# Kernel optimization log

Measured on AMD Instinct MI355X. Metric: run time of the kernel, lower is better.

The kernel has to match this reference:

```python
import jax, jax.numpy as jnp
import numpy as np

B, N, CIN, H, OUT, L, K = 8, 512, 64, 64, 64, 256, 3
EPS = 1e-5


def setup_inputs() -> dict:
    key = jax.random.key(0)
    ks = jax.random.split(key, 12)
    def unif(k, shape, fan):
        s = 1.0 / np.sqrt(fan)
        return jax.random.uniform(k, shape, jnp.float32, -s, s)
    return {
        "x": jax.random.normal(ks[0], (B, N, CIN, L), jnp.float32),
        "adj": jax.random.uniform(ks[1], (B, N, N), jnp.float32),
        # temp_conv1: Conv1d(CIN->H, k=3)
        "w1": unif(ks[2], (H, CIN, K), CIN * K),
        "b1": unif(ks[3], (H,), CIN * K),
        # graph_conv: Linear-style (H,H) + bias, stdv=1/sqrt(out_features)
        "gw": unif(ks[4], (H, H), H),
        "gb": unif(ks[5], (H,), H),
        # temp_conv2: Conv1d(H->OUT, k=3)
        "w2": unif(ks[6], (OUT, H, K), H * K),
        "b2": unif(ks[7], (OUT,), H * K),
        # residual: Conv1d(CIN->OUT, k=1) == pointwise linear
        "wr": unif(ks[8], (OUT, CIN), CIN),
        "br": unif(ks[9], (OUT,), CIN),
        # BatchNorm2d(OUT) affine params
        "gamma": jnp.ones((OUT,), jnp.float32),
        "beta": jnp.zeros((OUT,), jnp.float32),
    }


def _conv1d(x, w, b, pad):
    # x: (B, N, C, L) -> flatten node dim into batch, NCH conv
    b_, n_, c, l = x.shape
    y = jax.lax.conv_general_dilated(
        x.reshape(b_ * n_, c, l), w, window_strides=(1,),
        padding=[(pad, pad)], dimension_numbers=("NCH", "OIH", "NCH"))
    y = y + b[None, :, None]
    return y.reshape(b_, n_, w.shape[0], l)


def reference(x, adj, w1, b1, gw, gb, w2, b2, wr, br, gamma, beta):
    pad = (K - 1) // 2
    # residual branch: 1x1 conv over channels
    residual = jnp.einsum("bncl,oc->bnol", x, wr) + br[None, None, :, None]
    # temporal conv 1
    out = _conv1d(x, w1, b1, pad)                      # (B,N,H,L)
    # graph conv over all timesteps at once (replaces per-t Python loop)
    xw = jnp.einsum("bnhl,hd->bndl", out, gw)          # (B,N,H,L)
    out = jnp.einsum("bnm,bmdl->bndl", adj, xw) + gb[None, None, :, None]
    # temporal conv 2
    out = _conv1d(out, w2, b2, pad)                    # (B,N,OUT,L)
    out = out + residual
    # BatchNorm2d over channel axis (training-mode batch stats, biased var)
    mean = jnp.mean(out, axis=(0, 1, 3), keepdims=True)
    var = jnp.mean(jnp.square(out - mean), axis=(0, 1, 3), keepdims=True)
    out = (out - mean) * jax.lax.rsqrt(var + EPS)
    out = out * gamma[None, None, :, None] + beta[None, None, :, None]
    return jax.nn.relu(out)
```

## Files before the change

### kernel.cpp

```cpp
#include <hip/hip_runtime.h>
#include <hip/hip_bf16.h>
#include <stdint.h>


typedef unsigned short u16;
typedef unsigned int   u32;
typedef __attribute__((ext_vector_type(8))) short           bf16x8;
typedef __attribute__((ext_vector_type(8))) unsigned short  u16x8;
typedef __attribute__((ext_vector_type(4))) unsigned short  u16x4;
typedef __attribute__((ext_vector_type(4))) float           f32x4;

__device__ __forceinline__ float bf2f(u16 v){
  union { u32 u; float f; } x; x.u = ((u32)v) << 16; return x.f;
}
__device__ __forceinline__ u16 f2bf(float f){
  __hip_bfloat16 h = __float2bfloat16(f);
  return *reinterpret_cast<u16*>(&h);
}
__device__ __forceinline__ u32 swz(int row, int cbyte){
  return (u32)(row * 128) + (u32)(cbyte ^ ((row & 7) << 4));
}

__device__ __forceinline__ void stage_Tf(const float* __restrict__ src, u16* dst, int t){
  const int c0 = (t & 31) * 2;
  const int l0 = (t >> 5) * 32;
  #pragma unroll
  for (int v = 0; v < 8; ++v){
    f32x4 a = *(const f32x4*)(src + (size_t)c0 * 256 + l0 + v * 4);
    f32x4 b = *(const f32x4*)(src + (size_t)(c0 + 1) * 256 + l0 + v * 4);
    #pragma unroll
    for (int e = 0; e < 4; ++e){
      u32 p = (u32)f2bf(a[e]) | ((u32)f2bf(b[e]) << 16);
      *(u32*)((char*)dst + swz(l0 + v * 4 + e, c0 * 2)) = p;
    }
  }
}
__device__ __forceinline__ void stage_Tb(const u16* __restrict__ src, u16* dst, int t){
  const int c0 = (t & 31) * 2;
  const int l0 = (t >> 5) * 32;
  #pragma unroll
  for (int v = 0; v < 4; ++v){
    u16x8 a = *(const u16x8*)(src + (size_t)c0 * 256 + l0 + v * 8);
    u16x8 b = *(const u16x8*)(src + (size_t)(c0 + 1) * 256 + l0 + v * 8);
    #pragma unroll
    for (int e = 0; e < 8; ++e){
      u32 p = (u32)a[e] | ((u32)b[e] << 16);
      *(u32*)((char*)dst + swz(l0 + v * 8 + e, c0 * 2)) = p;
    }
  }
}

__global__ __launch_bounds__(256) void k_prep(const float* __restrict__ w1, const float* __restrict__ gw,
    const float* __restrict__ w2, const float* __restrict__ wr,
    u16* __restrict__ w1t, u16* __restrict__ gwt, u16* __restrict__ w2t, u16* __restrict__ wrt){
  int t = threadIdx.x;
  for (int e = t; e < 12288; e += 256){
    int tap = e >> 12, rem = e & 4095, o = rem >> 6, c = rem & 63;
    w1t[e] = f2bf(w1[(o * 64 + c) * 3 + tap]);
    w2t[e] = f2bf(w2[(o * 64 + c) * 3 + tap]);
  }
  for (int e = t; e < 4096; e += 256){
    int d = e >> 6, h = e & 63;
    gwt[e] = f2bf(gw[h * 64 + d]);
    wrt[e] = f2bf(wr[e]);
  }
}

__global__ __launch_bounds__(256) void k_p1(const float* __restrict__ x,
    const u16* __restrict__ w1t, const float* __restrict__ b1v,
    const u16* __restrict__ gwt, const u16* __restrict__ wrt,
    u16* __restrict__ outA, u16* __restrict__ outR){
  __shared__ u16 tile[16384];
  const int t = threadIdx.x;
  const size_t bn = (size_t)blockIdx.x + (size_t)blockIdx.y * 512;
  stage_Tf(x + bn * 16384, tile, t);
  __syncthreads();
  const int w = t >> 6, ln = t & 63, lq = ln >> 4, lr = ln & 15;
  const bf16x8 z8 = {};

  {
    f32x4 racc[4][4];
    #pragma unroll
    for (int i = 0; i < 4; ++i)
      #pragma unroll
      for (int j = 0; j < 4; ++j) racc[i][j] = (f32x4){0.f, 0.f, 0.f, 0.f};
    #pragma unroll
    for (int kk = 0; kk < 2; ++kk){
      bf16x8 A[4];
      #pragma unroll
      for (int fo = 0; fo < 4; ++fo)
        A[fo] = *(const bf16x8*)(wrt + (fo * 16 + lr) * 64 + kk * 32 + lq * 8);
      #pragma unroll
      for (int fc = 0; fc < 4; ++fc){
        int l = w * 64 + fc * 16 + lr;
        bf16x8 B = *(const bf16x8*)((char*)tile + swz(l, kk * 64 + lq * 16));
        #pragma unroll
        for (int fo = 0; fo < 4; ++fo)
          racc[fo][fc] = __builtin_amdgcn_mfma_f32_16x16x32_bf16(A[fo], B, racc[fo][fc], 0, 0, 0);
      }
    }
    u16* rp = outR + bn * 16384 + t * 64;
    #pragma unroll
    for (int v = 0; v < 8; ++v){
      u16x8 ov;
      const int fo = v >> 1;
      #pragma unroll
      for (int h = 0; h < 2; ++h){
        const int fc = (v & 1) * 2 + h;
        #pragma unroll
        for (int r2 = 0; r2 < 4; ++r2)
          ov[h * 4 + r2] = f2bf(racc[fo][fc][r2]);
      }
      *(u16x8*)(rp + v * 8) = ov;
    }
  }

  f32x4 acc[4][4];
  #pragma unroll
  for (int i = 0; i < 4; ++i)
    #pragma unroll
    for (int j = 0; j < 4; ++j) acc[i][j] = (f32x4){0.f, 0.f, 0.f, 0.f};
  #pragma unroll
  for (int tap = 0; tap < 3; ++tap){
    #pragma unroll
    for (int kk = 0; kk < 2; ++kk){
      bf16x8 A[4];
      #pragma unroll
      for (int fo = 0; fo < 4; ++fo)
        A[fo] = *(const bf16x8*)(w1t + tap * 4096 + (fo * 16 + lr) * 64 + kk * 32 + lq * 8);
      #pragma unroll
      for (int fc = 0; fc < 4; ++fc){
        int r = w * 64 + fc * 16 + lr + tap - 1;
        int rc = r < 0 ? 0 : (r > 255 ? 255 : r);
        bf16x8 B = *(const bf16x8*)((char*)tile + swz(rc, kk * 64 + lq * 16));
        if (r != rc) B = z8;
        #pragma unroll
        for (int fo = 0; fo < 4; ++fo)
          acc[fo][fc] = __builtin_amdgcn_mfma_f32_16x16x32_bf16(A[fo], B, acc[fo][fc], 0, 0, 0);
      }
    }
  }
  __syncthreads();
  #pragma unroll
  for (int fo = 0; fo < 4; ++fo){
    float b0 = b1v[fo * 16 + lq * 4 + 0];
    float b1_ = b1v[fo * 16 + lq * 4 + 1];
    float b2_ = b1v[fo * 16 + lq * 4 + 2];
    float b3 = b1v[fo * 16 + lq * 4 + 3];
    #pragma unroll
    for (int fc = 0; fc < 4; ++fc){
      int l = w * 64 + fc * 16 + lr;
      u32 p0 = (u32)f2bf(acc[fo][fc][0] + b0) | ((u32)f2bf(acc[fo][fc][1] + b1_) << 16);
      u32 p1 = (u32)f2bf(acc[fo][fc][2] + b2_) | ((u32)f2bf(acc[fo][fc][3] + b3) << 16);
      char* p = (char*)tile + swz(l, fo * 32 + lq * 8);
      *(u32*)p = p0;
      *(u32*)(p + 4) = p1;
    }
  }
  f32x4 acc2[4][4];
  #pragma unroll
  for (int i = 0; i < 4; ++i)
    #pragma unroll
    for (int j = 0; j < 4; ++j) acc2[i][j] = (f32x4){0.f, 0.f, 0.f, 0.f};
  #pragma unroll
  for (int kk = 0; kk < 2; ++kk){
    bf16x8 A[4];
    #pragma unroll
    for (int fo = 0; fo < 4; ++fo)
      A[fo] = *(const bf16x8*)(gwt + (fo * 16 + lr) * 64 + kk * 32 + lq * 8);
    #pragma unroll
    for (int fc = 0; fc < 4; ++fc){
      int l = w * 64 + fc * 16 + lr;
      bf16x8 B = *(const bf16x8*)((char*)tile + swz(l, kk * 64 + lq * 16));
      #pragma unroll
      for (int fo = 0; fo < 4; ++fo)
        acc2[fo][fc] = __builtin_amdgcn_mfma_f32_16x16x32_bf16(A[fo], B, acc2[fo][fc], 0, 0, 0);
    }
  }
  u16* op = outA + bn * 16384;
  #pragma unroll
  for (int fo = 0; fo < 4; ++fo)
    #pragma unroll
    for (int fc = 0; fc < 4; ++fc){
      int l = w * 64 + fc * 16 + lr;
      #pragma unroll
      for (int r2 = 0; r2 < 4; ++r2)
        op[(fo * 16 + lq * 4 + r2) * 256 + l] = f2bf(acc2[fo][fc][r2]);
    }
}

__global__ __launch_bounds__(256) void k_p3(const u16* __restrict__ xw,
    const float* __restrict__ adj, const float* __restrict__ gbv, u16* __restrict__ outB){
  __shared__ u16 At[8192];
  __shared__ u16 Bt[8192];
  const int t = threadIdx.x;
  const int jt = blockIdx.x, nt = blockIdx.y, b = blockIdx.z;
  const float* adjb = adj + ((size_t)b * 512 + (size_t)nt * 128) * 512;
  const u16* Xb = xw + (size_t)b * 8388608 + (size_t)jt * 128;
  const int w = t >> 6, ln = t & 63, lq = ln >> 4, lr = ln & 15;
  const int wrow = w >> 1, wcol = w & 1;
  const int mpair = t & 31, jq = t >> 5;
  f32x4 acc[4][4];
  #pragma unroll
  for (int i = 0; i < 4; ++i)
    #pragma unroll
    for (int j = 0; j < 4; ++j) acc[i][j] = (f32x4){0.f, 0.f, 0.f, 0.f};

  for (int ks = 0; ks < 8; ++ks){
    #pragma unroll
    for (int it = 0; it < 8; ++it){
      int c = it * 256 + t;
      int row = c >> 4, mc = c & 15;
      f32x4 v = *(const f32x4*)(adjb + (size_t)row * 512 + ks * 64 + mc * 4);
      u16x4 pk;
      #pragma unroll
      for (int e = 0; e < 4; ++e) pk[e] = f2bf(v[e]);
      *(u16x4*)((char*)At + (u32)(row * 128) + (u32)((mc * 8) ^ ((row & 7) << 4))) = pk;
    }
    {
      const u16* s0 = Xb + (size_t)(ks * 64 + mpair * 2) * 16384 + jq * 16;
      const u16* s1 = s0 + 16384;
      #pragma unroll
      for (int v2 = 0; v2 < 2; ++v2){
        u16x8 a = *(const u16x8*)(s0 + v2 * 8);
        u16x8 bb = *(const u16x8*)(s1 + v2 * 8);
        #pragma unroll
        for (int e = 0; e < 8; ++e){
          u32 p = (u32)a[e] | ((u32)bb[e] << 16);
          *(u32*)((char*)Bt + swz(jq * 16 + v2 * 8 + e, mpair * 4)) = p;
        }
      }
    }
    __syncthreads();
    #pragma unroll
    for (int kk = 0; kk < 2; ++kk){
      bf16x8 Af[4], Bf[4];
      #pragma unroll
      for (int f = 0; f < 4; ++f){
        int ra = wrow * 64 + f * 16 + lr;
        Af[f] = *(const bf16x8*)((char*)At + swz(ra, kk * 64 + lq * 16));
        int rb = wcol * 64 + f * 16 + lr;
        Bf[f] = *(const bf16x8*)((char*)Bt + swz(rb, kk * 64 + lq * 16));
      }
      #pragma unroll
      for (int fr = 0; fr < 4; ++fr)
        #pragma unroll
        for (int fc = 0; fc < 4; ++fc)
          acc[fr][fc] = __builtin_amdgcn_mfma_f32_16x16x32_bf16(Af[fr], Bf[fc], acc[fr][fc], 0, 0, 0);
    }
    __syncthreads();
  }
  const float gb = gbv[jt >> 1];
  u16* ob = outB + ((size_t)b * 512 + (size_t)nt * 128) * 16384 + (size_t)jt * 128;
  #pragma unroll
  for (int fr = 0; fr < 4; ++fr)
    #pragma unroll
    for (int fc = 0; fc < 4; ++fc)
      #pragma unroll
      for (int r2 = 0; r2 < 4; ++r2){
        int n_ = wrow * 64 + fr * 16 + lq * 4 + r2;
        int j_ = wcol * 64 + fc * 16 + lr;
        ob[(size_t)n_ * 16384 + j_] = f2bf(acc[fr][fc][r2] + gb);
      }
}

__global__ __launch_bounds__(256) void k_p4(const u16* __restrict__ g,
    const u16* __restrict__ resv, const u16* __restrict__ w2t,
    const float* __restrict__ b2v, const float* __restrict__ brv,
    u16* __restrict__ outP, float* __restrict__ spart){
  __shared__ u16 gt[16384];
  const int t = threadIdx.x;
  const size_t bn = (size_t)blockIdx.x + (size_t)blockIdx.y * 512;
  stage_Tb(g + bn * 16384, gt, t);
  __syncthreads();
  const int w = t >> 6, ln = t & 63, lq = ln >> 4, lr = ln & 15;
  const bf16x8 z8 = {};
  f32x4 acc[4][4];
  #pragma unroll
  for (int i = 0; i < 4; ++i)
    #pragma unroll
    for (int j = 0; j < 4; ++j) acc[i][j] = (f32x4){0.f, 0.f, 0.f, 0.f};

  #pragma unroll
  for (int tap = 0; tap < 3; ++tap){
    #pragma unroll
    for (int kk = 0; kk < 2; ++kk){
      bf16x8 A[4];
      #pragma unroll
      for (int fo = 0; fo < 4; ++fo)
        A[fo] = *(const bf16x8*)(w2t + tap * 4096 + (fo * 16 + lr) * 64 + kk * 32 + lq * 8);
      #pragma unroll
      for (int fc = 0; fc < 4; ++fc){
        int r = w * 64 + fc * 16 + lr + tap - 1;
        int rc = r < 0 ? 0 : (r > 255 ? 255 : r);
        bf16x8 B = *(const bf16x8*)((char*)gt + swz(rc, kk * 64 + lq * 16));
        if (r != rc) B = z8;
        #pragma unroll
        for (int fo = 0; fo < 4; ++fo)
          acc[fo][fc] = __builtin_amdgcn_mfma_f32_16x16x32_bf16(A[fo], B, acc[fo][fc], 0, 0, 0);
      }
    }
  }

  float bball[16];
  #pragma unroll
  for (int fo = 0; fo < 4; ++fo)
    #pragma unroll
    for (int r2 = 0; r2 < 4; ++r2){
      int o = fo * 16 + lq * 4 + r2;
      bball[fo * 4 + r2] = b2v[o] + brv[o];
    }
  float psum[16], psq[16];
  #pragma unroll
  for (int i = 0; i < 16; ++i){ psum[i] = 0.f; psq[i] = 0.f; }

  const u16* rp = resv + bn * 16384 + t * 64;
  u16x8 rv[8];
  #pragma unroll
  for (int v = 0; v < 8; ++v) rv[v] = *(const u16x8*)(rp + v * 8);

  u16* op = outP + bn * 16384;
  #pragma unroll
  for (int fo = 0; fo < 4; ++fo){
    #pragma unroll
    for (int fc = 0; fc < 4; ++fc){
      int l = w * 64 + fc * 16 + lr;
      #pragma unroll
      for (int r2 = 0; r2 < 4; ++r2){
        float val = acc[fo][fc][r2] + bball[fo * 4 + r2]
                  + bf2f(rv[fo * 2 + (fc >> 1)][(fc & 1) * 4 + r2]);
        op[(fo * 16 + lq * 4 + r2) * 256 + l] = f2bf(val);
        psum[fo * 4 + r2] += val;
        psq[fo * 4 + r2] += val * val;
      }
    }
  }

  #pragma unroll
  for (int i = 0; i < 16; ++i){
    #pragma unroll
    for (int m = 1; m < 16; m <<= 1){
      psum[i] += __shfl_xor(psum[i], m, 64);
      psq[i]  += __shfl_xor(psq[i],  m, 64);
    }
  }
  __syncthreads();
  float* sc = (float*)gt;
  if (lr == 0){
    #pragma unroll
    for (int i = 0; i < 16; ++i){
      int o = (i >> 2) * 16 + lq * 4 + (i & 3);
      sc[w * 128 + o]      = psum[i];
      sc[w * 128 + 64 + o] = psq[i];
    }
  }
  __syncthreads();
  if (t < 128){
    float tot = sc[t] + sc[128 + t] + sc[256 + t] + sc[384 + t];
    spart[(size_t)t * 4096 + bn] = tot;
  }
}

__global__ __launch_bounds__(256) void k_p5(const float* __restrict__ part, float* __restrict__ fin){
  const int o = blockIdx.x, t = threadIdx.x;
  float s1 = 0.f, s2 = 0.f;
  for (int k = t; k < 4096; k += 256){
    s1 += part[(size_t)o * 4096 + k];
    s2 += part[(size_t)(64 + o) * 4096 + k];
  }
  #pragma unroll
  for (int m = 32; m; m >>= 1){
    s1 += __shfl_down(s1, m, 64);
    s2 += __shfl_down(s2, m, 64);
  }
  __shared__ float red[8];
  if ((t & 63) == 0){ red[(t >> 6) * 2] = s1; red[(t >> 6) * 2 + 1] = s2; }
  __syncthreads();
  if (t == 0){
    float S1 = red[0] + red[2] + red[4] + red[6];
    float S2 = red[1] + red[3] + red[5] + red[7];
    const float invN = 1.f / 1048576.f;
    float mean = S1 * invN;
    float var = S2 * invN - mean * mean;
    fin[o] = mean;
    fin[64 + o] = rsqrtf(var + 1e-5f);
  }
}

__global__ __launch_bounds__(256) void k_p6(const u16* __restrict__ pre, const float* __restrict__ fin,
    const float* __restrict__ gamma, const float* __restrict__ beta, float* __restrict__ out){
  __shared__ float ssca[64], soff[64];
  const int tt = threadIdx.x;
  if (tt < 64){
    float sc = fin[64 + tt] * gamma[tt];
    ssca[tt] = sc;
    soff[tt] = beta[tt] - fin[tt] * sc;
  }
  __syncthreads();
  const size_t nchunk = 8388608;
  for (size_t i = (size_t)blockIdx.x * 256 + tt; i < nchunk; i += (size_t)gridDim.x * 256){
    int o = (int)((i >> 5) & 63);
    float sca = ssca[o], off = soff[o];
    u16x8 v = *(const u16x8*)(pre + i * 8);
    f32x4 oa, ob;
    #pragma unroll
    for (int e = 0; e < 4; ++e){
      float f0 = bf2f(v[e]) * sca + off;
      float f1 = bf2f(v[4 + e]) * sca + off;
      oa[e] = f0 > 0.f ? f0 : 0.f;
      ob[e] = f1 > 0.f ? f1 : 0.f;
    }
    *(f32x4*)(out + i * 8)     = oa;
    *(f32x4*)(out + i * 8 + 4) = ob;
  }
}

extern "C" void kernel_launch(void* const* d_in, const int* in_sizes, int n_in,
                              void* d_out, int out_size, void* d_ws, size_t ws_size,
                              hipStream_t stream){
  const float* x     = (const float*)d_in[0];
  const float* adj   = (const float*)d_in[1];
  const float* w1    = (const float*)d_in[2];
  const float* b1    = (const float*)d_in[3];
  const float* gw    = (const float*)d_in[4];
  const float* gb    = (const float*)d_in[5];
  const float* w2    = (const float*)d_in[6];
  const float* b2    = (const float*)d_in[7];
  const float* wr    = (const float*)d_in[8];
  const float* br    = (const float*)d_in[9];
  const float* gamma = (const float*)d_in[10];
  const float* beta  = (const float*)d_in[11];
  (void)in_sizes; (void)n_in; (void)out_size; (void)ws_size;

  char* ws = (char*)d_ws;
  u16*   bufA  = (u16*)ws;
  float* spart = (float*)(ws + 134217728);
  float* sfin  = (float*)(ws + 136314880);
  u16*   w1t   = (u16*)(ws + 136315392);
  u16*   gwt   = (u16*)(ws + 136339968);
  u16*   w2t   = (u16*)(ws + 136348160);
  u16*   wrt   = (u16*)(ws + 136372736);
  u16*   gbuf  = (u16*)d_out;
  u16*   bufR  = (u16*)d_out + 67108864;

  k_prep<<<1, 256, 0, stream>>>(w1, gw, w2, wr, w1t, gwt, w2t, wrt);
  k_p1<<<dim3(512, 8, 1), 256, 0, stream>>>(x, w1t, b1, gwt, wrt, bufA, bufR);
  k_p3<<<dim3(128, 4, 8), 256, 0, stream>>>(bufA, adj, gb, gbuf);
  k_p4<<<dim3(512, 8, 1), 256, 0, stream>>>(gbuf, bufR, w2t, b2, br, bufA, spart);
  k_p5<<<64, 256, 0, stream>>>(spart, sfin);
  k_p6<<<2048, 256, 0, stream>>>(bufA, sfin, gamma, beta, (float*)d_out);
}
```

Before: 587.7 us.

## Fold graph weight into conv1 weights and prefetch adjacency GEMM tiles

Precomputes gw^T·w1 per tap and b1·gw in the prep kernel, so k_p1 no longer needs its second GEMM, shared-memory round trip or extra barrier. The prep kernel now runs on 16 blocks. The adjacency GEMM kernel gets a flattened grid with a remapped block index to change scheduling locality across XCDs. It also prefetches the next K-slice of adj and xw into registers while the current slice is being multiplied. Folding the weights changes the rounding point (one bf16 rounding instead of two), and the prefetch raises register pressure.

```diff
diff --git a/kernel.cpp b/kernel.cpp
--- a/kernel.cpp
+++ b/kernel.cpp
@@ -50,26 +50,29 @@
   }
 }
 
-__global__ __launch_bounds__(256) void k_prep(const float* __restrict__ w1, const float* __restrict__ gw,
-    const float* __restrict__ w2, const float* __restrict__ wr,
-    u16* __restrict__ w1t, u16* __restrict__ gwt, u16* __restrict__ w2t, u16* __restrict__ wrt){
-  int t = threadIdx.x;
-  for (int e = t; e < 12288; e += 256){
+__global__ __launch_bounds__(256) void k_prep(const float* __restrict__ w1, const float* __restrict__ b1,
+    const float* __restrict__ gw, const float* __restrict__ w2, const float* __restrict__ wr,
+    u16* __restrict__ w1g, float* __restrict__ b1g, u16* __restrict__ w2t, u16* __restrict__ wrt){
+  const int gt = blockIdx.x * 256 + threadIdx.x, gs = gridDim.x * 256;
+  for (int e = gt; e < 12288; e += gs){
     int tap = e >> 12, rem = e & 4095, o = rem >> 6, c = rem & 63;
-    w1t[e] = f2bf(w1[(o * 64 + c) * 3 + tap]);
     w2t[e] = f2bf(w2[(o * 64 + c) * 3 + tap]);
-  }
-  for (int e = t; e < 4096; e += 256){
-    int d = e >> 6, h = e & 63;
-    gwt[e] = f2bf(gw[h * 64 + d]);
-    wrt[e] = f2bf(wr[e]);
+    float s = 0.f;
+    for (int h = 0; h < 64; ++h)
+      s += gw[h * 64 + o] * w1[(h * 64 + c) * 3 + tap];
+    w1g[e] = f2bf(s);
+  }
+  for (int e = gt; e < 4096; e += gs) wrt[e] = f2bf(wr[e]);
+  for (int d = gt; d < 64; d += gs){
+    float s = 0.f;
+    for (int h = 0; h < 64; ++h) s += b1[h] * gw[h * 64 + d];
+    b1g[d] = s;
   }
 }
 
 __global__ __launch_bounds__(256) void k_p1(const float* __restrict__ x,
-    const u16* __restrict__ w1t, const float* __restrict__ b1v,
-    const u16* __restrict__ gwt, const u16* __restrict__ wrt,
-    u16* __restrict__ outA, u16* __restrict__ outR){
+    const u16* __restrict__ w1g, const float* __restrict__ b1g,
+    const u16* __restrict__ wrt, u16* __restrict__ outA, u16* __restrict__ outR){
   __shared__ u16 tile[16384];
   const int t = threadIdx.x;
   const size_t bn = (size_t)blockIdx.x + (size_t)blockIdx.y * 512;
@@ -127,7 +130,7 @@
       bf16x8 A[4];
       #pragma unroll
       for (int fo = 0; fo < 4; ++fo)
-        A[fo] = *(const bf16x8*)(w1t + tap * 4096 + (fo * 16 + lr) * 64 + kk * 32 + lq * 8);
+        A[fo] = *(const bf16x8*)(w1g + tap * 4096 + (fo * 16 + lr) * 64 + kk * 32 + lq * 8);
       #pragma unroll
       for (int fc = 0; fc < 4; ++fc){
         int r = w * 64 + fc * 16 + lr + tap - 1;
@@ -140,53 +143,20 @@
       }
     }
   }
-  __syncthreads();
+  u16* op = outA + bn * 16384;
   #pragma unroll
   for (int fo = 0; fo < 4; ++fo){
-    float b0 = b1v[fo * 16 + lq * 4 + 0];
-    float b1_ = b1v[fo * 16 + lq * 4 + 1];
-    float b2_ = b1v[fo * 16 + lq * 4 + 2];
-    float b3 = b1v[fo * 16 + lq * 4 + 3];
+    float bb[4];
+    #pragma unroll
+    for (int r2 = 0; r2 < 4; ++r2) bb[r2] = b1g[fo * 16 + lq * 4 + r2];
     #pragma unroll
     for (int fc = 0; fc < 4; ++fc){
       int l = w * 64 + fc * 16 + lr;
-      u32 p0 = (u32)f2bf(acc[fo][fc][0] + b0) | ((u32)f2bf(acc[fo][fc][1] + b1_) << 16);
-      u32 p1 = (u32)f2bf(acc[fo][fc][2] + b2_) | ((u32)f2bf(acc[fo][fc][3] + b3) << 16);
-      char* p = (char*)tile + swz(l, fo * 32 + lq * 8);
-      *(u32*)p = p0;
-      *(u32*)(p + 4) = p1;
-    }
-  }
-  f32x4 acc2[4][4];
-  #pragma unroll
-  for (int i = 0; i < 4; ++i)
-    #pragma unroll
-    for (int j = 0; j < 4; ++j) acc2[i][j] = (f32x4){0.f, 0.f, 0.f, 0.f};
-  #pragma unroll
-  for (int kk = 0; kk < 2; ++kk){
-    bf16x8 A[4];
-    #pragma unroll
-    for (int fo = 0; fo < 4; ++fo)
-      A[fo] = *(const bf16x8*)(gwt + (fo * 16 + lr) * 64 + kk * 32 + lq * 8);
-    #pragma unroll
-    for (int fc = 0; fc < 4; ++fc){
-      int l = w * 64 + fc * 16 + lr;
-      bf16x8 B = *(const bf16x8*)((char*)tile + swz(l, kk * 64 + lq * 16));
-      #pragma unroll
-      for (int fo = 0; fo < 4; ++fo)
-        acc2[fo][fc] = __builtin_amdgcn_mfma_f32_16x16x32_bf16(A[fo], B, acc2[fo][fc], 0, 0, 0);
-    }
-  }
-  u16* op = outA + bn * 16384;
-  #pragma unroll
-  for (int fo = 0; fo < 4; ++fo)
-    #pragma unroll
-    for (int fc = 0; fc < 4; ++fc){
-      int l = w * 64 + fc * 16 + lr;
       #pragma unroll
       for (int r2 = 0; r2 < 4; ++r2)
-        op[(fo * 16 + lq * 4 + r2) * 256 + l] = f2bf(acc2[fo][fc][r2]);
-    }
+        op[(fo * 16 + lq * 4 + r2) * 256 + l] = f2bf(acc[fo][fc][r2] + bb[r2]);
+    }
+  }
 }
 
 __global__ __launch_bounds__(256) void k_p3(const u16* __restrict__ xw,
@@ -194,7 +164,8 @@
   __shared__ u16 At[8192];
   __shared__ u16 Bt[8192];
   const int t = threadIdx.x;
-  const int jt = blockIdx.x, nt = blockIdx.y, b = blockIdx.z;
+  const int wg = ((blockIdx.x & 7) << 9) | ((int)blockIdx.x >> 3);
+  const int jt = wg & 127, nt = (wg >> 7) & 3, b = wg >> 9;
   const float* adjb = adj + ((size_t)b * 512 + (size_t)nt * 128) * 512;
   const u16* Xb = xw + (size_t)b * 8388608 + (size_t)jt * 128;
   const int w = t >> 6, ln = t & 63, lq = ln >> 4, lr = ln & 15;
@@ -206,41 +177,54 @@
     #pragma unroll
     for (int j = 0; j < 4; ++j) acc[i][j] = (f32x4){0.f, 0.f, 0.f, 0.f};
 
-  for (int ks = 0; ks < 8; ++ks){
+  f32x4 ra[8];
+  u16x8 rb[4];
+  auto LOADK = [&](int ks){
     #pragma unroll
     for (int it = 0; it < 8; ++it){
       int c = it * 256 + t;
       int row = c >> 4, mc = c & 15;
-      f32x4 v = *(const f32x4*)(adjb + (size_t)row * 512 + ks * 64 + mc * 4);
+      ra[it] = *(const f32x4*)(adjb + (size_t)row * 512 + ks * 64 + mc * 4);
+    }
+    const u16* s0 = Xb + (size_t)(ks * 64 + mpair * 2) * 16384 + jq * 16;
+    const u16* s1 = s0 + 16384;
+    #pragma unroll
+    for (int v2 = 0; v2 < 2; ++v2){
+      rb[v2 * 2]     = *(const u16x8*)(s0 + v2 * 8);
+      rb[v2 * 2 + 1] = *(const u16x8*)(s1 + v2 * 8);
+    }
+  };
+
+  LOADK(0);
+  for (int ks = 0; ks < 8; ++ks){
+    #pragma unroll
+    for (int it = 0; it < 8; ++it){
+      int c = it * 256 + t;
+      int row = c >> 4, mc = c & 15;
       u16x4 pk;
       #pragma unroll
-      for (int e = 0; e < 4; ++e) pk[e] = f2bf(v[e]);
+      for (int e = 0; e < 4; ++e) pk[e] = f2bf(ra[it][e]);
       *(u16x4*)((char*)At + (u32)(row * 128) + (u32)((mc * 8) ^ ((row & 7) << 4))) = pk;
     }
-    {
-      const u16* s0 = Xb + (size_t)(ks * 64 + mpair * 2) * 16384 + jq * 16;
-      const u16* s1 = s0 + 16384;
-      #pragma unroll
-      for (int v2 = 0; v2 < 2; ++v2){
-        u16x8 a = *(const u16x8*)(s0 + v2 * 8);
-        u16x8 bb = *(const u16x8*)(s1 + v2 * 8);
-        #pragma unroll
-        for (int e = 0; e < 8; ++e){
-          u32 p = (u32)a[e] | ((u32)bb[e] << 16);
-          *(u32*)((char*)Bt + swz(jq * 16 + v2 * 8 + e, mpair * 4)) = p;
-        }
+    #pragma unroll
+    for (int v2 = 0; v2 < 2; ++v2){
+      #pragma unroll
+      for (int e = 0; e < 8; ++e){
+        u32 p = (u32)(u16)rb[v2 * 2][e] | ((u32)(u16)rb[v2 * 2 + 1][e] << 16);
+        *(u32*)((char*)Bt + swz(jq * 16 + v2 * 8 + e, mpair * 4)) = p;
       }
     }
     __syncthreads();
+    if (ks < 7) LOADK(ks + 1);
     #pragma unroll
     for (int kk = 0; kk < 2; ++kk){
       bf16x8 Af[4], Bf[4];
       #pragma unroll
       for (int f = 0; f < 4; ++f){
-        int ra = wrow * 64 + f * 16 + lr;
-        Af[f] = *(const bf16x8*)((char*)At + swz(ra, kk * 64 + lq * 16));
-        int rb = wcol * 64 + f * 16 + lr;
-        Bf[f] = *(const bf16x8*)((char*)Bt + swz(rb, kk * 64 + lq * 16));
+        int rA = wrow * 64 + f * 16 + lr;
+        Af[f] = *(const bf16x8*)((char*)At + swz(rA, kk * 64 + lq * 16));
+        int rB = wcol * 64 + f * 16 + lr;
+        Bf[f] = *(const bf16x8*)((char*)Bt + swz(rB, kk * 64 + lq * 16));
       }
       #pragma unroll
       for (int fr = 0; fr < 4; ++fr)
@@ -436,16 +420,16 @@
   u16*   bufA  = (u16*)ws;
   float* spart = (float*)(ws + 134217728);
   float* sfin  = (float*)(ws + 136314880);
-  u16*   w1t   = (u16*)(ws + 136315392);
-  u16*   gwt   = (u16*)(ws + 136339968);
+  u16*   w1g   = (u16*)(ws + 136315392);
+  float* b1g   = (float*)(ws + 136339968);
   u16*   w2t   = (u16*)(ws + 136348160);
   u16*   wrt   = (u16*)(ws + 136372736);
   u16*   gbuf  = (u16*)d_out;
   u16*   bufR  = (u16*)d_out + 67108864;
 
-  k_prep<<<1, 256, 0, stream>>>(w1, gw, w2, wr, w1t, gwt, w2t, wrt);
-  k_p1<<<dim3(512, 8, 1), 256, 0, stream>>>(x, w1t, b1, gwt, wrt, bufA, bufR);
-  k_p3<<<dim3(128, 4, 8), 256, 0, stream>>>(bufA, adj, gb, gbuf);
+  k_prep<<<16, 256, 0, stream>>>(w1, b1, gw, w2, wr, w1g, b1g, w2t, wrt);
+  k_p1<<<dim3(512, 8, 1), 256, 0, stream>>>(x, w1g, b1g, wrt, bufA, bufR);
+  k_p3<<<4096, 256, 0, stream>>>(bufA, adj, gb, gbuf);
   k_p4<<<dim3(512, 8, 1), 256, 0, stream>>>(gbuf, bufR, w2t, b2, br, bufA, spart);
   k_p5<<<64, 256, 0, stream>>>(spart, sfin);
   k_p6<<<2048, 256, 0, stream>>>(bufA, sfin, gamma, beta, (float*)d_out);
```

Measured after the change: 573.1 us. -2.5%, faster.
